# Kernel tuning notes

Measured on AMD Instinct MI355X. Metric: run time of the kernel, lower is better.

## Reference

```python
import jax, jax.numpy as jnp
import numpy as np

N = 50000        # bs * n_node
E = 800000       # n_edge
INPUT_NF = 64
HIDDEN_NF = 64
N_CHANNEL = 4
D = 3            # spatial dim
EDGE_D = 16
EPS = 1e-12      # F.normalize clamp


def _unif(k, shape, fan_in):
    s = 1.0 / np.sqrt(fan_in)
    return jax.random.uniform(k, shape, jnp.float32, -s, s)


def setup_inputs() -> dict:
    key = jax.random.key(0)
    ks = jax.random.split(key, 12)
    h = jax.random.normal(ks[0], (N, INPUT_NF), jnp.float32)
    coord = jax.random.normal(ks[1], (N, N_CHANNEL, D), jnp.float32)
    row = jax.random.randint(ks[2], (E,), 0, N)
    col = jax.random.randint(ks[3], (E,), 0, N)
    edge_attr = jax.random.normal(ks[4], (E, EDGE_D), jnp.float32)
    kv_in = INPUT_NF + N_CHANNEL * N_CHANNEL + EDGE_D
    Wq = _unif(ks[5], (INPUT_NF, HIDDEN_NF), INPUT_NF)
    bq = _unif(ks[6], (HIDDEN_NF,), INPUT_NF)
    Wkv = _unif(ks[7], (kv_in, 2 * HIDDEN_NF), kv_in)
    bkv = _unif(ks[8], (2 * HIDDEN_NF,), kv_in)
    W1 = _unif(ks[9], (HIDDEN_NF, HIDDEN_NF), HIDDEN_NF)
    b1 = _unif(ks[10], (HIDDEN_NF,), HIDDEN_NF)
    # xavier_uniform with gain=0.001, no bias
    lim = 0.001 * np.sqrt(6.0 / (HIDDEN_NF + N_CHANNEL))
    W2 = jax.random.uniform(ks[11], (HIDDEN_NF, N_CHANNEL), jnp.float32, -lim, lim)
    return dict(h=h, coord=coord, row=row, col=col, edge_attr=edge_attr,
                Wq=Wq, bq=bq, Wkv=Wkv, bkv=bkv, W1=W1, b1=b1, W2=W2)


def reference(h, coord, edge_attr, Wq, bq, Wkv, bkv, W1, b1, W2, row, col):
    n_node = h.shape[0]
    # coord2radial
    coord_diff = coord[row] - coord[col]                                # [E,C,D]
    radial = jnp.einsum('ecd,efd->ecf', coord_diff, coord_diff)         # [E,C,C]
    # F.normalize(radial, dim=0): L2-normalize across the edge dimension
    norm = jnp.maximum(jnp.sqrt(jnp.sum(radial * radial, axis=0, keepdims=True)), EPS)
    radial = radial / norm
    # att_model
    q = h[row] @ Wq + bq                                                # [E,H]
    target_feat = jnp.concatenate(
        [radial.reshape(radial.shape[0], -1), h[col], edge_attr], axis=1)
    kv = target_feat @ Wkv + bkv                                        # [E,2H]
    k, v = kv[:, 0::2], kv[:, 1::2]                                     # [E,H] each
    alpha = jnp.sum(q * k, axis=1)                                      # [E]
    # scatter_softmax over segments given by row (numerically stable)
    seg_max = jax.ops.segment_max(alpha, row, num_segments=n_node)
    ex = jnp.exp(alpha - seg_max[row])
    seg_sum = jax.ops.segment_sum(ex, row, num_segments=n_node)
    att = ex / seg_sum[row]                                             # [E]
    # node_model (dropout in eval mode = identity)
    h_out = h + jax.ops.segment_sum(att[:, None] * v, row, num_segments=n_node)
    # coord_model: coord_mlp = Linear -> SiLU -> Linear(no bias)
    coord_v = att[:, None] * (jax.nn.silu(v @ W1 + b1) @ W2)            # [E,C]
    trans = coord_diff * coord_v[:, :, None]                            # [E,C,D]
    coord_out = coord + jax.ops.segment_sum(trans, row, num_segments=n_node)
    return h_out, coord_out, att
```

## Files before the change

kernel.cpp:

```cpp
#include <hip/hip_runtime.h>
#include <math.h>

#define NN 50000
#define NE 800000
#define NPREB 1024

typedef __attribute__((ext_vector_type(8))) short short8;
typedef __attribute__((ext_vector_type(4))) float floatx4;

__device__ __forceinline__ unsigned short bf16_of(float x) {
  unsigned u = __float_as_uint(x);
  u += 0x7fffu + ((u >> 16) & 1u);
  return (unsigned short)(u >> 16);
}
__device__ __forceinline__ float bf2f(unsigned short u) {
  return __uint_as_float(((unsigned)u) << 16);
}
__device__ __forceinline__ unsigned pack_bf(float a, float b) {
  unsigned ua = __float_as_uint(a); ua += 0x7fffu + ((ua >> 16) & 1u);
  unsigned ub = __float_as_uint(b); ub += 0x7fffu + ((ub >> 16) & 1u);
  return (ua >> 16) | (ub & 0xffff0000u);
}
__device__ __forceinline__ float blo(unsigned w) { return __uint_as_float(w << 16); }
__device__ __forceinline__ float bhi(unsigned w) { return __uint_as_float(w & 0xffff0000u); }

__global__ __launch_bounds__(256)
void k_pre(const float* __restrict__ coord, const int* __restrict__ row,
           const int* __restrict__ col, const float* __restrict__ Wkv,
           const float* __restrict__ W1, const float* __restrict__ Wq,
           float* __restrict__ norm_part, int* __restrict__ deg,
           unsigned short* __restrict__ Bkvb, unsigned short* __restrict__ W1tb,
           unsigned* __restrict__ Wqp) {
  __shared__ float nred[4][16];
  const int gid = blockIdx.x * 256 + threadIdx.x;
  const int np = gridDim.x * 256;
  for (int idx = gid; idx < 128 * 96; idx += np) {
    int n = idx & 127, kk = idx >> 7;
    float w = (n < 64) ? Wkv[kk * 128 + 2 * n] : Wkv[kk * 128 + 2 * (n - 64) + 1];
    Bkvb[n * 104 + kk] = bf16_of(w);
  }
  for (int idx = gid; idx < 64 * 64; idx += np) {
    int n = idx & 63, kk = idx >> 6;
    W1tb[n * 88 + kk] = bf16_of(W1[kk * 64 + n]);
  }
  for (int idx = gid; idx < 32 * 64; idx += np) {
    int i2 = idx >> 6, j = idx & 63;
    Wqp[idx] = pack_bf(Wq[(2 * i2) * 64 + j], Wq[(2 * i2 + 1) * 64 + j]);
  }
  float accv[16];
#pragma unroll
  for (int j = 0; j < 16; ++j) accv[j] = 0.f;
  for (int e = gid; e < NE; e += np) {
    int r = row[e], c = col[e];
    const float4* cr = (const float4*)(coord + (size_t)r * 12);
    const float4* cc = (const float4*)(coord + (size_t)c * 12);
    float cd[12];
#pragma unroll
    for (int q = 0; q < 3; ++q) {
      float4 a = cr[q], b = cc[q];
      cd[q * 4 + 0] = a.x - b.x; cd[q * 4 + 1] = a.y - b.y;
      cd[q * 4 + 2] = a.z - b.z; cd[q * 4 + 3] = a.w - b.w;
    }
#pragma unroll
    for (int c4 = 0; c4 < 4; ++c4)
#pragma unroll
      for (int f4 = 0; f4 < 4; ++f4) {
        float v = cd[c4 * 3] * cd[f4 * 3] + cd[c4 * 3 + 1] * cd[f4 * 3 + 1] +
                  cd[c4 * 3 + 2] * cd[f4 * 3 + 2];
        accv[c4 * 4 + f4] += v * v;
      }
    atomicAdd(deg + r, 1);
  }
  const int lane = threadIdx.x & 63, wvb = threadIdx.x >> 6;
#pragma unroll
  for (int j = 0; j < 16; ++j) {
    accv[j] += __shfl_xor(accv[j], 1);
    accv[j] += __shfl_xor(accv[j], 2);
    accv[j] += __shfl_xor(accv[j], 4);
    accv[j] += __shfl_xor(accv[j], 8);
    accv[j] += __shfl_xor(accv[j], 16);
    accv[j] += __shfl_xor(accv[j], 32);
  }
  if (lane == 0) {
#pragma unroll
    for (int j = 0; j < 16; ++j) nred[wvb][j] = accv[j];
  }
  __syncthreads();
  if (threadIdx.x < 16) {
    float s = nred[0][threadIdx.x] + nred[1][threadIdx.x] +
              nred[2][threadIdx.x] + nred[3][threadIdx.x];
    norm_part[blockIdx.x * 16 + threadIdx.x] = s;
  }
}

__global__ __launch_bounds__(1024)
void k_scanq(const int* __restrict__ deg, int* __restrict__ cursor,
             const float* __restrict__ norm_part, float* __restrict__ rnorm,
             const float* __restrict__ h, const unsigned* __restrict__ Wqp,
             const float* __restrict__ bq,
             unsigned short* __restrict__ qg2, unsigned short* __restrict__ hb) {
  __shared__ int part[1024];
  __shared__ float nr[64][16];
  __shared__ float sHr[16][64];
  const int t = threadIdx.x;
  if (blockIdx.x == 0) {
    {
      const int i = t >> 4, c = t & 15;
      float s = 0.f;
#pragma unroll
      for (int j = 0; j < NPREB / 64; ++j) s += norm_part[((i + 64 * j) << 4) + c];
      nr[i][c] = s;
    }
    __syncthreads();
    if (t < 16) {
      float s = 0.f;
#pragma unroll 8
      for (int i = 0; i < 64; ++i) s += nr[i][t];
      rnorm[t] = 1.0f / fmaxf(sqrtf(s), 1e-12f);
    }
    const int CH = (NN + 1023) / 1024;
    const int lo = t * CH, hi = (lo + CH < NN) ? lo + CH : NN;
    int s = 0;
    for (int i = lo; i < hi; ++i) s += deg[i];
    part[t] = s;
    __syncthreads();
    for (int off = 1; off < 1024; off <<= 1) {
      int v = (t >= off) ? part[t - off] : 0;
      __syncthreads();
      part[t] += v;
      __syncthreads();
    }
    int base = (t == 0) ? 0 : part[t - 1];
    for (int i = lo; i < hi; ++i) {
      cursor[i] = base; base += deg[i];
    }
    return;
  }
  const int wv = t >> 6, lane = t & 63;
  const int node = (blockIdx.x - 1) * 16 + wv;
  float hv = h[(size_t)node * 64 + lane];
  sHr[wv][lane] = hv;
  hb[(size_t)node * 64 + lane] = bf16_of(hv);
  float q = bq[lane];
  const float2* hp = (const float2*)sHr[wv];
#pragma unroll 8
  for (int i2 = 0; i2 < 32; ++i2) {
    unsigned w = Wqp[i2 * 64 + lane];
    float2 hbv = hp[i2];
    q += hbv.x * blo(w) + hbv.y * bhi(w);
  }
  qg2[(size_t)node * 64 + (lane & 15) * 4 + (lane >> 4)] = bf16_of(q);
}

__global__ void k_scatter(const int* __restrict__ row, const int* __restrict__ col,
                          const float* __restrict__ edge_attr,
                          int* __restrict__ cursor, int* __restrict__ iperm,
                          unsigned* __restrict__ rcp, uint4* __restrict__ eab) {
  int e = blockIdx.x * 256 + threadIdx.x;
  if (e < NE) {
    int r = row[e], c = col[e];
    int p = atomicAdd(cursor + r, 1);
    iperm[e] = p;
    rcp[p] = ((unsigned)r << 16) | (unsigned)c;
    const float4* ep = (const float4*)(edge_attr + (size_t)e * 16);
    float4 f0 = ep[0], f1 = ep[1], f2 = ep[2], f3 = ep[3];
    uint4 a, b;
    a.x = pack_bf(f0.x, f0.y); a.y = pack_bf(f0.z, f0.w);
    a.z = pack_bf(f1.x, f1.y); a.w = pack_bf(f1.z, f1.w);
    b.x = pack_bf(f2.x, f2.y); b.y = pack_bf(f2.z, f2.w);
    b.z = pack_bf(f3.x, f3.y); b.w = pack_bf(f3.z, f3.w);
    eab[(size_t)p * 2]     = a;
    eab[(size_t)p * 2 + 1] = b;
  }
}

__global__ __launch_bounds__(512, 6)
void k_kv(const unsigned short* __restrict__ hb, const float* __restrict__ coord,
          const float* __restrict__ bkv, const float* __restrict__ b1,
          const float* __restrict__ W2, const float* __restrict__ rnorm,
          const unsigned* __restrict__ rcp, const uint4* __restrict__ eab,
          const unsigned short* __restrict__ Bkvb,
          const unsigned short* __restrict__ W1tb,
          const unsigned short* __restrict__ qg2,
          float* __restrict__ exg, float* __restrict__ l_g,
          float* __restrict__ hacc_g, float* __restrict__ cacc_g) {
  __shared__ __align__(16) unsigned short sA[128][104];
  __shared__ __align__(16) unsigned short sB[128][104];
  __shared__ unsigned sRC[128];
  unsigned short (*sW1t)[88] = (unsigned short (*)[88])&sB[0][0];

  const int tid = threadIdx.x;
  const int base = blockIdx.x * 128;

  const uint4* gw = (const uint4*)W1tb;
  uint4 w1a = gw[tid];
  uint4 w1b;
  if (tid < 192) w1b = gw[512 + tid];

  if (tid < 128) sRC[tid] = rcp[base + tid];
  if (tid < 256) {
    int s = tid >> 1;
    *(uint4*)&sA[s][80 + (tid & 1) * 8] = eab[(size_t)base * 2 + tid];
  }
  for (int idx = tid; idx < 1024; idx += 512) {
    int s = idx >> 3, k8 = idx & 7;
    unsigned c = rcp[base + s] & 0xffffu;
    uint4 u = ((const uint4*)(hb + (size_t)c * 64))[k8];
    *(uint4*)&sA[s][16 + k8 * 8] = u;
  }
  {
    const uint4* gb = (const uint4*)Bkvb;
    uint4* sb = (uint4*)&sB[0][0];
    for (int idx = tid; idx < 1664; idx += 512) sb[idx] = gb[idx];
  }
  const int wv = tid >> 6, lane = tid & 63;
  float cdp[4];
  {
    const int grp = lane >> 4, g = lane & 15;
    const int c4 = g >> 2, f4 = g & 3;
    const float rn = rnorm[g];
#pragma unroll
    for (int it = 0; it < 4; ++it) {
      int slot = 16 * wv + it * 4 + grp;
      unsigned rc = rcp[base + slot];
      int r = (int)(rc >> 16), c = (int)(rc & 0xffffu);
      float cd = 0.f;
      if (g < 12) cd = coord[r * 12 + g] - coord[c * 12 + g];
      cdp[it] = cd;
      float rad = 0.f;
#pragma unroll
      for (int d = 0; d < 3; ++d)
        rad += __shfl(cd, grp * 16 + c4 * 3 + d) * __shfl(cd, grp * 16 + f4 * 3 + d);
      sA[slot][g] = bf16_of(rad * rn);
    }
  }
  __syncthreads();

  const int m16 = lane & 15, quad = lane >> 4;
  const int arow = 16 * wv + m16;

  floatx4 acc[8];
#pragma unroll
  for (int i = 0; i < 8; ++i) acc[i] = (floatx4){0.f, 0.f, 0.f, 0.f};
#pragma unroll
  for (int ks = 0; ks < 3; ++ks) {
    short8 af = *(const short8*)&sA[arow][ks * 32 + quad * 8];
#pragma unroll
    for (int nt = 0; nt < 8; ++nt) {
      short8 bf = *(const short8*)&sB[nt * 16 + m16][ks * 32 + quad * 8];
      acc[nt] = __builtin_amdgcn_mfma_f32_16x16x32_bf16(af, bf, acc[nt], 0, 0, 0);
    }
  }
#pragma unroll
  for (int nt = 0; nt < 4; ++nt) {
    float bk = bkv[2 * (m16 + 16 * nt)];
    float bv = bkv[2 * (m16 + 16 * nt) + 1];
#pragma unroll
    for (int r = 0; r < 4; ++r) { acc[nt][r] += bk; acc[nt + 4][r] += bv; }
  }
  float part[4] = {0.f, 0.f, 0.f, 0.f};
#pragma unroll
  for (int r = 0; r < 4; ++r) {
    unsigned nrow = sRC[16 * wv + quad * 4 + r] >> 16;
    uint2 qp = *(const uint2*)(qg2 + (size_t)nrow * 64 + m16 * 4);
    part[r] += blo(qp.x) * acc[0][r] + bhi(qp.x) * acc[1][r] +
               blo(qp.y) * acc[2][r] + bhi(qp.y) * acc[3][r];
  }
#pragma unroll
  for (int off = 1; off < 16; off <<= 1) {
#pragma unroll
    for (int r = 0; r < 4; ++r) part[r] += __shfl_xor(part[r], off);
  }
  float ex[4];
#pragma unroll
  for (int r = 0; r < 4; ++r) ex[r] = __expf(part[r]);
  if (m16 == 0) {
#pragma unroll
    for (int r = 0; r < 4; ++r)
      exg[base + 16 * wv + quad * 4 + r] = ex[r];
  }
#pragma unroll
  for (int nt = 0; nt < 4; ++nt)
#pragma unroll
    for (int r = 0; r < 4; ++r)
      sA[16 * wv + quad * 4 + r][m16 + 16 * nt] = bf16_of(acc[4 + nt][r]);
#pragma unroll
  for (int it = 0; it < 4; ++it)
    if (m16 < 12) sA[16 * wv + it * 4 + quad][64 + m16] = bf16_of(cdp[it]);

  __syncthreads();
  {
    unsigned short* sw = &sB[0][0];
    *(uint4*)&sw[(size_t)tid * 8] = w1a;
    if (tid < 192) *(uint4*)&sw[(size_t)(512 + tid) * 8] = w1b;
  }
  __syncthreads();

  floatx4 tacc[4];
#pragma unroll
  for (int i = 0; i < 4; ++i) tacc[i] = (floatx4){0.f, 0.f, 0.f, 0.f};
#pragma unroll
  for (int ks = 0; ks < 2; ++ks) {
    short8 af = *(const short8*)&sA[arow][ks * 32 + quad * 8];
#pragma unroll
    for (int nt = 0; nt < 4; ++nt) {
      short8 bf = *(const short8*)&sW1t[nt * 16 + m16][ks * 32 + quad * 8];
      tacc[nt] = __builtin_amdgcn_mfma_f32_16x16x32_bf16(af, bf, tacc[nt], 0, 0, 0);
    }
  }
#pragma unroll
  for (int nt = 0; nt < 4; ++nt) {
    float bb = b1[m16 + 16 * nt];
#pragma unroll
    for (int r = 0; r < 4; ++r) {
      float t = tacc[nt][r] + bb;
      tacc[nt][r] = t * __builtin_amdgcn_rcpf(1.f + __expf(-t));
    }
  }
  float w0[16];
#pragma unroll
  for (int r = 0; r < 4; ++r)
#pragma unroll
    for (int c = 0; c < 4; ++c) w0[r * 4 + c] = 0.f;
#pragma unroll
  for (int nt = 0; nt < 4; ++nt) {
    float4 w2r = ((const float4*)W2)[m16 + 16 * nt];
#pragma unroll
    for (int r = 0; r < 4; ++r) {
      w0[r * 4 + 0] += tacc[nt][r] * w2r.x;
      w0[r * 4 + 1] += tacc[nt][r] * w2r.y;
      w0[r * 4 + 2] += tacc[nt][r] * w2r.z;
      w0[r * 4 + 3] += tacc[nt][r] * w2r.w;
    }
  }
  float rs1[8];
#pragma unroll
  for (int jj = 0; jj < 8; ++jj) {
    float snd = (m16 & 8) ? w0[jj] : w0[jj + 8];
    float rcv = __shfl_xor(snd, 8);
    rs1[jj] = ((m16 & 8) ? w0[jj + 8] : w0[jj]) + rcv;
  }
  float rs2[4];
#pragma unroll
  for (int jj = 0; jj < 4; ++jj) {
    float snd = (m16 & 4) ? rs1[jj] : rs1[jj + 4];
    float rcv = __shfl_xor(snd, 4);
    rs2[jj] = ((m16 & 4) ? rs1[jj + 4] : rs1[jj]) + rcv;
  }
  float rs3[2];
#pragma unroll
  for (int jj = 0; jj < 2; ++jj) {
    float snd = (m16 & 2) ? rs2[jj] : rs2[jj + 2];
    float rcv = __shfl_xor(snd, 2);
    rs3[jj] = ((m16 & 2) ? rs2[jj + 2] : rs2[jj]) + rcv;
  }
  float cvtot;
  {
    float snd = (m16 & 1) ? rs3[0] : rs3[1];
    float rcv = __shfl_xor(snd, 1);
    cvtot = ((m16 & 1) ? rs3[1] : rs3[0]) + rcv;
  }
  const int d3 = (m16 < 12) ? ((m16 * 11) >> 5) : 3;
  float tr[4];
#pragma unroll
  for (int r = 0; r < 4; ++r) {
    float cvv = __shfl(cvtot, (quad << 4) + r * 4 + d3);
    tr[r] = (m16 < 12) ? bf2f(sA[16 * wv + quad * 4 + r][64 + m16]) * cvv : 0.f;
  }

  int s = 0;
  while (s < 16) {
    int n = (int)(sRC[16 * wv + s] >> 16);
    int e2 = s + 1;
    while (e2 < 16 && (int)(sRC[16 * wv + e2] >> 16) == n) ++e2;
    float hp0 = 0.f, hp1 = 0.f, hp2 = 0.f, hp3 = 0.f, lp = 0.f, cp = 0.f;
#pragma unroll
    for (int r = 0; r < 4; ++r) {
      int rowi = quad * 4 + r;
      float w = (rowi >= s && rowi < e2) ? ex[r] : 0.f;
      hp0 += w * acc[4][r];
      hp1 += w * acc[5][r];
      hp2 += w * acc[6][r];
      hp3 += w * acc[7][r];
      lp  += (rowi >= s && rowi < e2) ? ex[r] : 0.f;
      cp  += w * tr[r];
    }
    hp0 += __shfl_xor(hp0, 16); hp0 += __shfl_xor(hp0, 32);
    hp1 += __shfl_xor(hp1, 16); hp1 += __shfl_xor(hp1, 32);
    hp2 += __shfl_xor(hp2, 16); hp2 += __shfl_xor(hp2, 32);
    hp3 += __shfl_xor(hp3, 16); hp3 += __shfl_xor(hp3, 32);
    lp  += __shfl_xor(lp, 16);  lp  += __shfl_xor(lp, 32);
    cp  += __shfl_xor(cp, 16);  cp  += __shfl_xor(cp, 32);
    if (quad == 0) {
      float* hg = hacc_g + (size_t)n * 64;
      atomicAdd(hg + m16,      hp0);
      atomicAdd(hg + m16 + 16, hp1);
      atomicAdd(hg + m16 + 32, hp2);
      atomicAdd(hg + m16 + 48, hp3);
      if (m16 < 12) atomicAdd(cacc_g + (size_t)n * 12 + m16, cp);
      if (m16 == 0) atomicAdd(l_g + n, lp);
    }
    s = e2;
  }
}

__global__ __launch_bounds__(256)
void k_fin(const float* __restrict__ h, const float* __restrict__ coord,
           const int* __restrict__ row, const int* __restrict__ iperm,
           const float* __restrict__ exg, const float* __restrict__ l_g,
           const float* __restrict__ hacc_g, const float* __restrict__ cacc_g,
           float* __restrict__ out) {
  const int node = blockIdx.x * 16 + (threadIdx.x >> 4);
  const int q16 = threadIdx.x & 15;
  const float l = l_g[node];
  const float inv = (l > 0.f) ? 1.f / l : 0.f;
  {
    float4 hv = ((const float4*)(h + (size_t)node * 64))[q16];
    float4 av = ((const float4*)(hacc_g + (size_t)node * 64))[q16];
    float4 o;
    o.x = hv.x + av.x * inv; o.y = hv.y + av.y * inv;
    o.z = hv.z + av.z * inv; o.w = hv.w + av.w * inv;
    ((float4*)(out + (size_t)node * 64))[q16] = o;
  }
  if (q16 < 3) {
    float4 cv = ((const float4*)(coord + (size_t)node * 12))[q16];
    float4 av = ((const float4*)(cacc_g + (size_t)node * 12))[q16];
    float4 o;
    o.x = cv.x + av.x * inv; o.y = cv.y + av.y * inv;
    o.z = cv.z + av.z * inv; o.w = cv.w + av.w * inv;
    ((float4*)(out + (size_t)NN * 64 + (size_t)node * 12))[q16] = o;
  }
  const int e = blockIdx.x * 256 + threadIdx.x;
  float le = l_g[row[e]];
  out[(size_t)NN * 64 + NN * 12 + e] = exg[iperm[e]] * __builtin_amdgcn_rcpf(le);
}

extern "C" void kernel_launch(void* const* d_in, const int* in_sizes, int n_in,
                              void* d_out, int out_size, void* d_ws, size_t ws_size,
                              hipStream_t stream) {
  const float* h         = (const float*)d_in[0];
  const float* coord     = (const float*)d_in[1];
  const int*   row       = (const int*)d_in[2];
  const int*   col       = (const int*)d_in[3];
  const float* edge_attr = (const float*)d_in[4];
  const float* Wq        = (const float*)d_in[5];
  const float* bq        = (const float*)d_in[6];
  const float* Wkv       = (const float*)d_in[7];
  const float* bkv       = (const float*)d_in[8];
  const float* W1        = (const float*)d_in[9];
  const float* b1        = (const float*)d_in[10];
  const float* W2        = (const float*)d_in[11];
  float* out = (float*)d_out;

  size_t off = 0;
  char* wsb = (char*)d_ws;
  auto alloc = [&](size_t bytes) {
    off = (off + 255) & ~(size_t)255;
    void* p = wsb + off; off += bytes; return p;
  };
  int*            deg      = (int*)alloc((size_t)NN * 4);
  float*          l_g      = (float*)alloc((size_t)NN * 4);
  float*          hacc_g   = (float*)alloc((size_t)NN * 64 * 4);
  float*          cacc_g   = (float*)alloc((size_t)NN * 12 * 4);
  size_t zbytes = off;
  float*          norm_part= (float*)alloc((size_t)NPREB * 16 * 4);
  float*          rnorm    = (float*)alloc(16 * 4);
  int*            cursor   = (int*)alloc((size_t)NN * 4);
  unsigned*       rcp      = (unsigned*)alloc((size_t)NE * 4);
  int*            iperm    = (int*)alloc((size_t)NE * 4);
  float*          exg      = (float*)alloc((size_t)NE * 4);
  uint4*          eab      = (uint4*)alloc((size_t)NE * 32);
  unsigned short* qg2      = (unsigned short*)alloc((size_t)NN * 64 * 2);
  unsigned short* hb       = (unsigned short*)alloc((size_t)NN * 64 * 2);
  unsigned short* Bkvb     = (unsigned short*)alloc(128 * 104 * 2);
  unsigned short* W1tb     = (unsigned short*)alloc(64 * 88 * 2);
  unsigned*       Wqp      = (unsigned*)alloc(32 * 64 * 4);

  hipMemsetAsync(d_ws, 0, zbytes, stream);

  k_pre<<<NPREB, 256, 0, stream>>>(coord, row, col, Wkv, W1, Wq,
                                   norm_part, deg, Bkvb, W1tb, Wqp);
  k_scanq<<<1 + NN / 16, 1024, 0, stream>>>(deg, cursor, norm_part,
                                            rnorm, h, Wqp, bq, qg2, hb);
  k_scatter<<<(NE + 255) / 256, 256, 0, stream>>>(row, col, edge_attr, cursor,
                                                  iperm, rcp, eab);
  k_kv<<<NE / 128, 512, 0, stream>>>(hb, coord, bkv, b1, W2, rnorm,
                                     rcp, eab, Bkvb, W1tb, qg2,
                                     exg, l_g, hacc_g, cacc_g);
  k_fin<<<NN / 16, 256, 0, stream>>>(h, coord, row, iperm, exg, l_g,
                                     hacc_g, cacc_g, out);
}
```

Before: 430.6 us.

## Compute node query projection with MFMA bf16 tiles in scan kernel

Replaces the per-lane scalar dot-product loop for q = h@Wq+bq with 16x16x32 bf16 MFMA instructions, each wave handling 16 nodes instead of one. Wq is pre-transposed to bf16 for the B operand. h is staged as bf16 in shared memory and loaded with float4 vectors, and the grid shrinks by 16x. The goal is to cut ALU and load instruction count in this kernel. h is now rounded to bf16 before the projection, which slightly changes q precision.

```diff
diff --git a/kernel.cpp b/kernel.cpp
--- a/kernel.cpp
+++ b/kernel.cpp
@@ -30,7 +30,7 @@
            const float* __restrict__ W1, const float* __restrict__ Wq,
            float* __restrict__ norm_part, int* __restrict__ deg,
            unsigned short* __restrict__ Bkvb, unsigned short* __restrict__ W1tb,
-           unsigned* __restrict__ Wqp) {
+           unsigned short* __restrict__ Wqtb) {
   __shared__ float nred[4][16];
   const int gid = blockIdx.x * 256 + threadIdx.x;
   const int np = gridDim.x * 256;
@@ -43,9 +43,9 @@
     int n = idx & 63, kk = idx >> 6;
     W1tb[n * 88 + kk] = bf16_of(W1[kk * 64 + n]);
   }
-  for (int idx = gid; idx < 32 * 64; idx += np) {
-    int i2 = idx >> 6, j = idx & 63;
-    Wqp[idx] = pack_bf(Wq[(2 * i2) * 64 + j], Wq[(2 * i2 + 1) * 64 + j]);
+  for (int idx = gid; idx < 64 * 64; idx += np) {
+    int n = idx & 63, kk = idx >> 6;
+    Wqtb[n * 64 + kk] = bf16_of(Wq[kk * 64 + n]);
   }
   float accv[16];
 #pragma unroll
@@ -96,12 +96,12 @@
 __global__ __launch_bounds__(1024)
 void k_scanq(const int* __restrict__ deg, int* __restrict__ cursor,
              const float* __restrict__ norm_part, float* __restrict__ rnorm,
-             const float* __restrict__ h, const unsigned* __restrict__ Wqp,
+             const float* __restrict__ h, const unsigned short* __restrict__ Wqtb,
              const float* __restrict__ bq,
              unsigned short* __restrict__ qg2, unsigned short* __restrict__ hb) {
   __shared__ int part[1024];
   __shared__ float nr[64][16];
-  __shared__ float sHr[16][64];
+  __shared__ __align__(16) unsigned short sH[16][16][72];
   const int t = threadIdx.x;
   if (blockIdx.x == 0) {
     {
@@ -137,19 +137,41 @@
     return;
   }
   const int wv = t >> 6, lane = t & 63;
-  const int node = (blockIdx.x - 1) * 16 + wv;
-  float hv = h[(size_t)node * 64 + lane];
-  sHr[wv][lane] = hv;
-  hb[(size_t)node * 64 + lane] = bf16_of(hv);
-  float q = bq[lane];
-  const float2* hp = (const float2*)sHr[wv];
-#pragma unroll 8
-  for (int i2 = 0; i2 < 32; ++i2) {
-    unsigned w = Wqp[i2 * 64 + lane];
-    float2 hbv = hp[i2];
-    q += hbv.x * blo(w) + hbv.y * bhi(w);
-  }
-  qg2[(size_t)node * 64 + (lane & 15) * 4 + (lane >> 4)] = bf16_of(q);
+  const int nbase = (blockIdx.x - 1) * 256 + wv * 16;
+  if (nbase >= NN) return;
+  const float4* hsrc = (const float4*)(h + (size_t)nbase * 64);
+#pragma unroll
+  for (int i = 0; i < 4; ++i) {
+    int fi = i * 64 + lane;
+    int nd = fi >> 4, c4 = fi & 15;
+    float4 v = hsrc[fi];
+    uint2 u; u.x = pack_bf(v.x, v.y); u.y = pack_bf(v.z, v.w);
+    *(uint2*)&sH[wv][nd][c4 * 4] = u;
+    *(uint2*)&hb[((size_t)nbase + nd) * 64 + c4 * 4] = u;
+  }
+  const int m16 = lane & 15, quad = lane >> 4;
+  floatx4 acc[4];
+#pragma unroll
+  for (int i = 0; i < 4; ++i) acc[i] = (floatx4){0.f, 0.f, 0.f, 0.f};
+#pragma unroll
+  for (int ks = 0; ks < 2; ++ks) {
+    short8 af = *(const short8*)&sH[wv][m16][ks * 32 + quad * 8];
+#pragma unroll
+    for (int nt = 0; nt < 4; ++nt) {
+      short8 bf = *(const short8*)&Wqtb[(nt * 16 + m16) * 64 + ks * 32 + quad * 8];
+      acc[nt] = __builtin_amdgcn_mfma_f32_16x16x32_bf16(af, bf, acc[nt], 0, 0, 0);
+    }
+  }
+  const float bq0 = bq[m16], bq1 = bq[16 + m16];
+  const float bq2 = bq[32 + m16], bq3 = bq[48 + m16];
+#pragma unroll
+  for (int r = 0; r < 4; ++r) {
+    size_t nd = (size_t)nbase + quad * 4 + r;
+    uint2 u;
+    u.x = pack_bf(acc[0][r] + bq0, acc[1][r] + bq1);
+    u.y = pack_bf(acc[2][r] + bq2, acc[3][r] + bq3);
+    *(uint2*)&qg2[nd * 64 + m16 * 4] = u;
+  }
 }
 
 __global__ void k_scatter(const int* __restrict__ row, const int* __restrict__ col,
@@ -474,14 +496,14 @@
   unsigned short* hb       = (unsigned short*)alloc((size_t)NN * 64 * 2);
   unsigned short* Bkvb     = (unsigned short*)alloc(128 * 104 * 2);
   unsigned short* W1tb     = (unsigned short*)alloc(64 * 88 * 2);
-  unsigned*       Wqp      = (unsigned*)alloc(32 * 64 * 4);
+  unsigned short* Wqtb     = (unsigned short*)alloc(64 * 64 * 2);
 
   hipMemsetAsync(d_ws, 0, zbytes, stream);
 
   k_pre<<<NPREB, 256, 0, stream>>>(coord, row, col, Wkv, W1, Wq,
-                                   norm_part, deg, Bkvb, W1tb, Wqp);
-  k_scanq<<<1 + NN / 16, 1024, 0, stream>>>(deg, cursor, norm_part,
-                                            rnorm, h, Wqp, bq, qg2, hb);
+                                   norm_part, deg, Bkvb, W1tb, Wqtb);
+  k_scanq<<<1 + (NN + 255) / 256, 1024, 0, stream>>>(deg, cursor, norm_part,
+                                                     rnorm, h, Wqtb, bq, qg2, hb);
   k_scatter<<<(NE + 255) / 256, 256, 0, stream>>>(row, col, edge_attr, cursor,
                                                   iperm, rcp, eab);
   k_kv<<<NE / 128, 512, 0, stream>>>(hb, coord, bkv, b1, W2, rnorm,
```

Result: no change. 429.9 us (-0.2%).
